# Kernel optimization log

Hardware: AMD Instinct MI355X
Metric: run time of the kernel (lower is better)

The kernel has to match this reference:

```python
import jax, jax.numpy as jnp
import numpy as np

VSIZE = 100000
LENGTH = 200
BATCH = 1024

def setup_inputs() -> dict:
    key = jax.random.key(0)
    k1, k2, k3 = jax.random.split(key, 3)
    x = jax.random.randint(k1, (LENGTH, BATCH), 0, VSIZE, dtype=jnp.int64)
    # nn.Linear(vsize, 1): weight (1, vsize), bias (1,)
    bound = 1.0 / np.sqrt(VSIZE)
    W = jax.random.uniform(k2, (1, VSIZE), minval=-bound, maxval=bound, dtype=jnp.float32)
    b_lut = jax.random.uniform(k3, (1,), minval=-bound, maxval=bound, dtype=jnp.float32)
    bias = jnp.zeros((1,), dtype=jnp.float32)
    return {"x": x, "W": W, "b_lut": b_lut, "bias": bias}

def reference(x, W, b_lut, bias):
    # x: (length, batch) int token ids.
    # Original builds a (vsize, batch) presence indicator ((counts > 0).float())
    # then applies Linear(vsize, 1). Equivalent: presence[b, v] = 1 if token v
    # appears in column b, out[b] = presence[b] . W[0] + b_lut + bias.
    length, batch = x.shape
    bi = jnp.broadcast_to(jnp.arange(batch), (length, batch))
    presence = jnp.zeros((batch, VSIZE), dtype=jnp.float32).at[bi, x].set(1.0)
    out = presence @ W[0] + b_lut[0] + bias[0]  # (batch,)
    return out
```

## Files before the change

kernel.cpp:

```cpp
#include <hip/hip_runtime.h>


#define VSIZE     100000
#define LENGTH    200
#define BATCH     1024
#define HASH_SIZE 1024
#define EMPTY     0xFFFFFFFFu

__global__ __launch_bounds__(256) void LR2_kernel(
    const int* __restrict__ x,
    const float* __restrict__ W,
    const float* __restrict__ b_lut,
    const float* __restrict__ bias,
    float* __restrict__ out)
{
    __shared__ unsigned ht[HASH_SIZE];
    __shared__ float    wsum[4];

    const int b = blockIdx.x;
    const int t = threadIdx.x;

    unsigned tok = EMPTY;
    float    w   = 0.0f;
    if (t < LENGTH) {
        tok = (unsigned)x[t * BATCH + b];
        w   = W[tok];
    }
    const float tail = b_lut[0] + bias[0];

    ((uint4*)ht)[t] = make_uint4(EMPTY, EMPTY, EMPTY, EMPTY);
    __syncthreads();

    float contrib = 0.0f;
    if (t < LENGTH) {
        unsigned h = (tok * 2654435761u) >> 22;
        for (;;) {
            unsigned old = atomicCAS(&ht[h], EMPTY, tok);
            if (old == EMPTY) { contrib = w; break; }
            if (old == tok) break;
            h = (h + 1) & (HASH_SIZE - 1);
        }
    }

    for (int off = 32; off > 0; off >>= 1)
        contrib += __shfl_down(contrib, off, 64);

    const int wave = t >> 6;
    if ((t & 63) == 0) wsum[wave] = contrib;
    __syncthreads();

    if (t == 0)
        out[b] = wsum[0] + wsum[1] + wsum[2] + wsum[3] + tail;
}

extern "C" void kernel_launch(void* const* d_in, const int* in_sizes, int n_in,
                              void* d_out, int out_size, void* d_ws, size_t ws_size,
                              hipStream_t stream) {
    const int*   x     = (const int*)d_in[0];
    const float* W     = (const float*)d_in[1];
    const float* b_lut = (const float*)d_in[2];
    const float* bias  = (const float*)d_in[3];
    float*       out   = (float*)d_out;

    LR2_kernel<<<BATCH, 256, 0, stream>>>(x, W, b_lut, bias, out);
}
```

Measured before the change: 9.572 us.

## Use one wavefront per batch column with four tokens per lane

The block shrinks from 256 threads to a single 64-lane wavefront. Each lane now loads up to four token ids and their weights, initializes four hash-table slots, and inserts its tokens into the shared hash one after another. With only one wave per block, the shared-memory partial-sum array and both __syncthreads barriers go away, and the wave reduction writes the output directly. The cost is fewer threads in flight to hide gather latency, and hash insertions that run serially within each lane.

```diff
diff --git a/kernel.cpp b/kernel.cpp
--- a/kernel.cpp
+++ b/kernel.cpp
@@ -7,7 +7,7 @@
 #define HASH_SIZE 1024
 #define EMPTY     0xFFFFFFFFu
 
-__global__ __launch_bounds__(256) void LR2_kernel(
+__global__ __launch_bounds__(64) void LR2_kernel(
     const int* __restrict__ x,
     const float* __restrict__ W,
     const float* __restrict__ b_lut,
@@ -15,29 +15,40 @@
     float* __restrict__ out)
 {
     __shared__ unsigned ht[HASH_SIZE];
-    __shared__ float    wsum[4];
 
-    const int b = blockIdx.x;
-    const int t = threadIdx.x;
+    const int b    = blockIdx.x;
+    const int lane = threadIdx.x;
 
-    unsigned tok = EMPTY;
-    float    w   = 0.0f;
-    if (t < LENGTH) {
-        tok = (unsigned)x[t * BATCH + b];
-        w   = W[tok];
+    const int ntok = (lane < (LENGTH - 192)) ? 4 : 3;
+
+    unsigned tok[4];
+    float    w[4];
+    #pragma unroll
+    for (int k = 0; k < 4; ++k) {
+        tok[k] = EMPTY;
+        w[k]   = 0.0f;
+        if (k < ntok) tok[k] = (unsigned)x[(lane + 64 * k) * BATCH + b];
     }
+    #pragma unroll
+    for (int k = 0; k < 4; ++k)
+        if (k < ntok) w[k] = W[tok[k]];
+
     const float tail = b_lut[0] + bias[0];
 
-    ((uint4*)ht)[t] = make_uint4(EMPTY, EMPTY, EMPTY, EMPTY);
-    __syncthreads();
+    uint4* htv = (uint4*)ht;
+    #pragma unroll
+    for (int k = 0; k < 4; ++k)
+        htv[lane + 64 * k] = make_uint4(EMPTY, EMPTY, EMPTY, EMPTY);
 
     float contrib = 0.0f;
-    if (t < LENGTH) {
-        unsigned h = (tok * 2654435761u) >> 22;
+    #pragma unroll
+    for (int k = 0; k < 4; ++k) {
+        if (k >= ntok) continue;
+        unsigned h = (tok[k] * 2654435761u) >> 22;
         for (;;) {
-            unsigned old = atomicCAS(&ht[h], EMPTY, tok);
-            if (old == EMPTY) { contrib = w; break; }
-            if (old == tok) break;
+            unsigned old = atomicCAS(&ht[h], EMPTY, tok[k]);
+            if (old == EMPTY) { contrib += w[k]; break; }
+            if (old == tok[k]) break;
             h = (h + 1) & (HASH_SIZE - 1);
         }
     }
@@ -45,12 +56,7 @@
     for (int off = 32; off > 0; off >>= 1)
         contrib += __shfl_down(contrib, off, 64);
 
-    const int wave = t >> 6;
-    if ((t & 63) == 0) wsum[wave] = contrib;
-    __syncthreads();
-
-    if (t == 0)
-        out[b] = wsum[0] + wsum[1] + wsum[2] + wsum[3] + tail;
+    if (lane == 0) out[b] = contrib + tail;
 }
 
 extern "C" void kernel_launch(void* const* d_in, const int* in_sizes, int n_in,
@@ -62,5 +68,5 @@
     const float* bias  = (const float*)d_in[3];
     float*       out   = (float*)d_out;
 
-    LR2_kernel<<<BATCH, 256, 0, stream>>>(x, W, b_lut, bias, out);
+    LR2_kernel<<<BATCH, 64, 0, stream>>>(x, W, b_lut, bias, out);
 }
```

Result: no change. 9.655 us (+0.9%).
